# Optimization experiments

Measured on AMD Instinct MI355X. Metric: run time of the kernel, lower is better.

## Reference

```python
import jax, jax.numpy as jnp
import numpy as np

N = 100000   # nodes
E = 1600000  # edges
IN, HID, CLS = 128, 64, 32


def gcn_conv(x, src, dst, W, b, num_nodes):
    """PyG-style GCNConv: out = D^{-1/2} (A+I) D^{-1/2} X W + b."""
    xw = x @ W  # transform first (matches PyG: propagate on transformed feats)
    loop = jnp.arange(num_nodes)
    src_f = jnp.concatenate([src, loop])
    dst_f = jnp.concatenate([dst, loop])
    ones = jnp.ones(src_f.shape[0], dtype=xw.dtype)
    deg = jax.ops.segment_sum(ones, dst_f, num_segments=num_nodes)
    dinv = jnp.where(deg > 0, jax.lax.rsqrt(deg), 0.0)
    norm = dinv[src_f] * dinv[dst_f]            # [E+N]
    msg = xw[src_f] * norm[:, None]             # gather + scale
    out = jax.ops.segment_sum(msg, dst_f, num_segments=num_nodes)
    return out + b


def setup_inputs() -> dict:
    key = jax.random.key(0)
    k = jax.random.split(key, 7)
    x = jax.random.normal(k[0], (N, IN), dtype=jnp.float32)
    edge_index = jax.random.randint(k[1], (2, E), 0, N)
    edge_attr = jax.random.normal(k[2], (E, 1), dtype=jnp.float32)
    W1 = jax.random.normal(k[3], (IN, HID), dtype=jnp.float32) / np.sqrt(IN)
    b1 = jnp.zeros((HID,), dtype=jnp.float32)
    W2 = jax.random.normal(k[4], (HID, CLS), dtype=jnp.float32) / np.sqrt(HID)
    b2 = jnp.zeros((CLS,), dtype=jnp.float32)
    return {"x": x, "edge_index": edge_index, "edge_attr": edge_attr,
            "W1": W1, "b1": b1, "W2": W2, "b2": b2}


def reference(x, edge_index, edge_attr, W1, b1, W2, b2):
    # edge_attr is unpacked by the original forward but unused by GCNConv
    src, dst = edge_index[0], edge_index[1]
    h = jax.nn.relu(gcn_conv(x, src, dst, W1, b1, N))
    return gcn_conv(h, src, dst, W2, b2, N)
```

## Files before the change

### kernel.cpp

```cpp
#include <hip/hip_runtime.h>
#include <hip/hip_fp16.h>

#define N_NODES 100000
#define N_EDGES 1600000
#define IN_F 128
#define HID_F 64
#define CLS_F 32

#define NBKT 512
#define BKT_NODES 196
#define EPB 16384
#define NBLK 98
#define NVAL (NBKT * NBLK)
#define CAPB 5120

typedef short s8v __attribute__((ext_vector_type(8)));
typedef float f4v __attribute__((ext_vector_type(4)));

__device__ __forceinline__ unsigned short f2h(float f) {
    return __half_as_ushort(__float2half_rn(f));
}
__device__ __forceinline__ int packh2(float x, float y) {
    __half2 p = __floats2half2_rn(x, y);
    union { __half2 h; int i; } c; c.h = p; return c.i;
}
__device__ __forceinline__ void acc8(float* a, int4 v) {
    union { int4 i; __half2 h[4]; } c; c.i = v;
#pragma unroll
    for (int j = 0; j < 4; j++) {
        float2 f = __half22float2(c.h[j]);
        a[2 * j] += f.x;
        a[2 * j + 1] += f.y;
    }
}
__device__ __forceinline__ void acc4(float* a, int2 v) {
    union { int2 i; __half2 h[2]; } c; c.i = v;
#pragma unroll
    for (int j = 0; j < 2; j++) {
        float2 f = __half22float2(c.h[j]);
        a[2 * j] += f.x;
        a[2 * j + 1] += f.y;
    }
}


__global__ __launch_bounds__(256) void bucketA_kernel(const int* __restrict__ dst,
                                                      int* __restrict__ bh) {
    __shared__ int h[NBKT];
    for (int i = threadIdx.x; i < NBKT; i += 256) h[i] = 0;
    __syncthreads();
    int e0 = blockIdx.x * EPB;
    int e1 = min(e0 + EPB, N_EDGES);
    for (int e = e0 + threadIdx.x; e < e1; e += 256)
        atomicAdd(&h[dst[e] / BKT_NODES], 1);
    __syncthreads();
    for (int i = threadIdx.x; i < NBKT; i += 256)
        bh[i * NBLK + blockIdx.x] = h[i];
}

__global__ __launch_bounds__(1024) void scan_hist_kernel(int* __restrict__ bh) {
    __shared__ int wsum[16];
    const int CH = (NVAL + 1023) / 1024;
    int t = threadIdx.x;
    int base = t * CH;
    int v[CH];
    int local = 0;
#pragma unroll
    for (int i = 0; i < CH; i++) {
        int idx = base + i;
        int x = (idx < NVAL) ? bh[idx] : 0;
        v[i] = local;
        local += x;
    }
    int lane = t & 63, w = t >> 6;
    int s = local;
#pragma unroll
    for (int d = 1; d < 64; d <<= 1) {
        int u = __shfl_up(s, d);
        if (lane >= d) s += u;
    }
    if (lane == 63) wsum[w] = s;
    __syncthreads();
    int wbase = 0;
    for (int i = 0; i < w; i++) wbase += wsum[i];
    int tbase = wbase + s - local;
#pragma unroll
    for (int i = 0; i < CH; i++) {
        int idx = base + i;
        if (idx < NVAL) bh[idx] = tbase + v[i];
    }
}

__global__ __launch_bounds__(256) void bucketB_kernel(const int* __restrict__ src,
                                                      const int* __restrict__ dst,
                                                      const int* __restrict__ bhScan,
                                                      unsigned* __restrict__ bkt) {
    __shared__ int cur[NBKT];
    for (int i = threadIdx.x; i < NBKT; i += 256)
        cur[i] = bhScan[i * NBLK + blockIdx.x];
    __syncthreads();
    int e0 = blockIdx.x * EPB;
    int e1 = min(e0 + EPB, N_EDGES);
    for (int e = e0 + threadIdx.x; e < e1; e += 256) {
        int d = dst[e];
        int g = d / BKT_NODES;
        unsigned pk = ((unsigned)(d - g * BKT_NODES) << 17) | (unsigned)src[e];
        int pos = atomicAdd(&cur[g], 1);
        bkt[pos] = pk;
    }
}

__global__ __launch_bounds__(256) void sort_bucket_kernel(const int* __restrict__ bhScan,
                                                          const unsigned* __restrict__ bkt,
                                                          int* __restrict__ csr,
                                                          int* __restrict__ off,
                                                          int* __restrict__ endp,
                                                          float* __restrict__ dinv) {
    __shared__ int hist[BKT_NODES];
    __shared__ int loff[BKT_NODES];
    __shared__ int loffB[BKT_NODES];
    __shared__ int wt[4];
    __shared__ int csrS[CAPB];
    int b = blockIdx.x;
    int t = threadIdx.x;
    int s0 = bhScan[b * NBLK];
    int s1 = (b < NBKT - 1) ? bhScan[(b + 1) * NBLK] : N_EDGES;
    int nE = s1 - s0;

    for (int i = t; i < BKT_NODES; i += 256) hist[i] = 0;
    __syncthreads();
    for (int i = t; i < nE; i += 256)
        atomicAdd(&hist[bkt[s0 + i] >> 17], 1);
    __syncthreads();

    int h0 = 0, h1 = 0;
    if (t < 98) { h0 = hist[2 * t]; h1 = hist[2 * t + 1]; }
    int p0 = (h0 + 7) & ~7;
    int p1 = (h1 + 7) & ~7;
    int sum = p0 + p1;
    int lane = t & 63, w = t >> 6;
    int s = sum;
#pragma unroll
    for (int d = 1; d < 64; d <<= 1) {
        int u = __shfl_up(s, d);
        if (lane >= d) s += u;
    }
    if (lane == 63) wt[w] = s;
    __syncthreads();
    int wbase = 0;
    for (int i = 0; i < w; i++) wbase += wt[i];
    int excl = wbase + s - sum;
    if (t < 98) {
        loff[2 * t] = excl;         loffB[2 * t] = excl;
        loff[2 * t + 1] = excl + p0; loffB[2 * t + 1] = excl + p0;
    }
    __syncthreads();

    for (int j = t; j < BKT_NODES; j += 256) {
        int n = b * BKT_NODES + j;
        if (n < N_NODES) {
            int c = hist[j];
            int o = b * CAPB + loff[j];
            off[n] = o;
            endp[n] = o + ((c + 7) & ~7);
            dinv[n] = rsqrtf((float)(c + 1));
        }
    }
    __syncthreads();

    for (int i = t; i < nE; i += 256) {
        unsigned pk = bkt[s0 + i];
        int dl = (int)(pk >> 17);
        int p = atomicAdd(&loff[dl], 1);
        csrS[p] = (int)(pk & 0x1FFFFu);
    }
    __syncthreads();

    for (int j = t; j < BKT_NODES; j += 256) {
        int c = hist[j];
        int bse = loffB[j];
        int pe = bse + ((c + 7) & ~7);
        for (int p = bse + c; p < pe; p++) csrS[p] = N_NODES;
    }
    __syncthreads();

    int padTot = wt[0] + wt[1] + wt[2] + wt[3];
    for (int i = t; i < padTot; i += 256) csr[b * CAPB + i] = csrS[i];
}

#define XBM 64
__global__ __launch_bounds__(256) void xw1_kernel(const float* __restrict__ x,
                                                  const float* __restrict__ W1,
                                                  const float* __restrict__ dinv,
                                                  unsigned short* __restrict__ y1h) {
    __shared__ __align__(16) unsigned short Wb[16 * 64 * 8];
    __shared__ __align__(16) unsigned short xb[XBM][IN_F + 8];

    int tid = threadIdx.x;

    for (int i = tid; i < IN_F * HID_F; i += 256) {
        int k = i >> 6, n = i & 63;
        int kc = k >> 5, kw = k & 31;
        int nt = n >> 4, nl = n & 15;
        int quad = kw >> 3, j = kw & 7;
        Wb[(((kc * 4 + nt) * 64) + quad * 16 + nl) * 8 + j] = f2h(W1[i]);
    }

    int nodeBase = blockIdx.x * XBM;
    {
        int snl = tid >> 2;
        int sk0 = (tid & 3) * 32;
        int n = nodeBase + snl;
#pragma unroll
        for (int kk = 0; kk < 32; kk += 4) {
            float4 v = make_float4(0.f, 0.f, 0.f, 0.f);
            if (n < N_NODES) v = *(const float4*)(x + (size_t)n * IN_F + sk0 + kk);
            ushort4 o;
            o.x = f2h(v.x); o.y = f2h(v.y); o.z = f2h(v.z); o.w = f2h(v.w);
            *(ushort4*)(&xb[snl][sk0 + kk]) = o;
        }
    }
    __syncthreads();

    int wave = tid >> 6, lane = tid & 63;
    int quad = lane >> 4, l15 = lane & 15;
    int rowBase = wave * 16;

    f4v acc[4];
#pragma unroll
    for (int i = 0; i < 4; i++) acc[i] = (f4v){0.f, 0.f, 0.f, 0.f};

#pragma unroll
    for (int kc = 0; kc < 4; kc++) {
        s8v a = *(const s8v*)(&xb[rowBase + l15][kc * 32 + quad * 8]);
#pragma unroll
        for (int nt = 0; nt < 4; nt++) {
            s8v b = *(const s8v*)(&Wb[((kc * 4 + nt) * 64 + lane) * 8]);
            acc[nt] = __builtin_amdgcn_mfma_f32_16x16x32_f16(a, b, acc[nt], 0, 0, 0);
        }
    }

    float dv[4];
    int n0 = nodeBase + rowBase + quad * 4;
#pragma unroll
    for (int r = 0; r < 4; r++)
        dv[r] = (n0 + r < N_NODES) ? dinv[n0 + r] : 0.f;
#pragma unroll
    for (int nt = 0; nt < 4; nt++) {
#pragma unroll
        for (int r = 0; r < 4; r++) {
            int n = n0 + r;
            if (n < N_NODES + 1)
                y1h[(size_t)n * HID_F + nt * 16 + l15] = f2h(acc[nt][r] * dv[r]);
        }
    }
}

__global__ __launch_bounds__(256) void gather1_kernel(
        const int* __restrict__ off, const int* __restrict__ endp,
        const int* __restrict__ csr, const unsigned short* __restrict__ y1h,
        const float* __restrict__ dinv, const float* __restrict__ b1,
        unsigned short* __restrict__ hout) {
    int tid = threadIdx.x;
    int wv = __builtin_amdgcn_readfirstlane(tid >> 6);
    int wave = blockIdx.x * 4 + wv;
    int nA = wave * 2, nB = nA + 1;
    int lane = tid & 63;
    int f = lane & 7;
    int g = lane >> 3;
    int fo = f * 16;

    int offA = off[nA], offB = off[nB];
    int lenA = endp[nA] - offA, lenB = endp[nB] - offB;
    const int* pA = csr + offA + g;
    const int* pB = csr + offB + g;
    const char* yb = (const char*)y1h;

    float aA[8], aB[8];
#pragma unroll
    for (int j = 0; j < 8; j++) { aA[j] = 0.f; aB[j] = 0.f; }

    int lmin = min(lenA, lenB);
    int iA = pA[0], iB = pB[0];
    int t = 0;
    for (; t < lmin; t += 8) {
        int icA = iA, icB = iB;
        iA = pA[t + 8]; iB = pB[t + 8];
        int4 vA = *(const int4*)(yb + (size_t)icA * 128 + fo);
        int4 vB = *(const int4*)(yb + (size_t)icB * 128 + fo);
        acc8(aA, vA); acc8(aB, vB);
    }
    for (; t < lenA; t += 8) {
        int ic = iA; iA = pA[t + 8];
        int4 v = *(const int4*)(yb + (size_t)ic * 128 + fo);
        acc8(aA, v);
    }
    for (int u = lmin; u < lenB; u += 8) {
        int ic = iB; iB = pB[u + 8];
        int4 v = *(const int4*)(yb + (size_t)ic * 128 + fo);
        acc8(aB, v);
    }

#pragma unroll
    for (int m = 8; m <= 32; m <<= 1) {
#pragma unroll
        for (int j = 0; j < 8; j++) {
            aA[j] += __shfl_xor(aA[j], m);
            aB[j] += __shfl_xor(aB[j], m);
        }
    }

    int4 sA = *(const int4*)(yb + (size_t)nA * 128 + fo);
    int4 sB = *(const int4*)(yb + (size_t)nB * 128 + fo);
    acc8(aA, sA); acc8(aB, sB);

    float dvA = dinv[nA], dvB = dinv[nB];
    float4 bl = *(const float4*)(b1 + 8 * f);
    float4 bh4 = *(const float4*)(b1 + 8 * f + 4);
    float bb[8] = {bl.x, bl.y, bl.z, bl.w, bh4.x, bh4.y, bh4.z, bh4.w};
    float hA[8], hB[8];
#pragma unroll
    for (int j = 0; j < 8; j++) {
        hA[j] = fmaxf(aA[j] * dvA + bb[j], 0.f);
        hB[j] = fmaxf(aB[j] * dvB + bb[j], 0.f);
    }
    int4 HA, HB;
    HA.x = packh2(hA[0], hA[1]); HA.y = packh2(hA[2], hA[3]);
    HA.z = packh2(hA[4], hA[5]); HA.w = packh2(hA[6], hA[7]);
    HB.x = packh2(hB[0], hB[1]); HB.y = packh2(hB[2], hB[3]);
    HB.z = packh2(hB[4], hB[5]); HB.w = packh2(hB[6], hB[7]);

    if (lane < 16) {
        int node = (lane < 8) ? nA : nB;
        int4 hv = (lane < 8) ? HA : HB;
        *(int4*)((char*)hout + (size_t)node * 128 + (lane & 7) * 16) = hv;
    }
}

#define YBM 64
__global__ __launch_bounds__(256) void y2_kernel(const unsigned short* __restrict__ h,
                                                 const float* __restrict__ W2,
                                                 const float* __restrict__ dinv,
                                                 unsigned short* __restrict__ y2h) {
    __shared__ __align__(16) unsigned short Wb[2 * 2 * 64 * 8];
    __shared__ __align__(16) unsigned short hb[YBM][HID_F + 8];
    int tid = threadIdx.x;

    for (int i = tid; i < HID_F * CLS_F; i += 256) {
        int k = i >> 5, n = i & 31;
        int kc = k >> 5, kw = k & 31;
        int nt = n >> 4, nl = n & 15;
        int quad = kw >> 3, j = kw & 7;
        Wb[(((kc * 2 + nt) * 64) + quad * 16 + nl) * 8 + j] = f2h(W2[i]);
    }

    int nodeBase = blockIdx.x * YBM;
    {
        int row = tid >> 2, sseg = tid & 3;
        int n = nodeBase + row;
        int4 v0 = {0, 0, 0, 0}, v1 = {0, 0, 0, 0};
        if (n < N_NODES) {
            const char* hp = (const char*)h + (size_t)n * 128 + sseg * 32;
            v0 = *(const int4*)hp;
            v1 = *(const int4*)(hp + 16);
        }
        *(int4*)(&hb[row][sseg * 16]) = v0;
        *(int4*)(&hb[row][sseg * 16 + 8]) = v1;
    }
    __syncthreads();

    int wave = tid >> 6, lane = tid & 63;
    int quad = lane >> 4, l15 = lane & 15;
    int rowBase = wave * 16;

    f4v acc[2];
#pragma unroll
    for (int i = 0; i < 2; i++) acc[i] = (f4v){0.f, 0.f, 0.f, 0.f};

#pragma unroll
    for (int kc = 0; kc < 2; kc++) {
        s8v a = *(const s8v*)(&hb[rowBase + l15][kc * 32 + quad * 8]);
#pragma unroll
        for (int nt = 0; nt < 2; nt++) {
            s8v b = *(const s8v*)(&Wb[((kc * 2 + nt) * 64 + lane) * 8]);
            acc[nt] = __builtin_amdgcn_mfma_f32_16x16x32_f16(a, b, acc[nt], 0, 0, 0);
        }
    }

    float dv[4];
    int n0 = nodeBase + rowBase + quad * 4;
#pragma unroll
    for (int r = 0; r < 4; r++)
        dv[r] = (n0 + r < N_NODES) ? dinv[n0 + r] : 0.f;
#pragma unroll
    for (int nt = 0; nt < 2; nt++) {
#pragma unroll
        for (int r = 0; r < 4; r++) {
            int n = n0 + r;
            if (n < N_NODES + 1)
                y2h[(size_t)n * CLS_F + nt * 16 + l15] = f2h(acc[nt][r] * dv[r]);
        }
    }
}

__global__ __launch_bounds__(256) void gather2_kernel(const int* __restrict__ off,
                                                      const int* __restrict__ endp,
                                                      const int* __restrict__ csr,
                                                      const unsigned short* __restrict__ y2h,
                                                      const float* __restrict__ dinv,
                                                      const float* __restrict__ b2,
                                                      float* __restrict__ out) {
    int tid = threadIdx.x;
    int wv = __builtin_amdgcn_readfirstlane(tid >> 6);
    int wave = blockIdx.x * 4 + wv;
    int nA = wave * 2, nB = nA + 1;
    int lane = tid & 63;
    int f = lane & 7;
    int g = lane >> 3;
    int fo = f * 8;

    int offA = off[nA], offB = off[nB];
    int lenA = endp[nA] - offA, lenB = endp[nB] - offB;
    const int* pA = csr + offA + g;
    const int* pB = csr + offB + g;
    const char* yb = (const char*)y2h;

    float aA[4], aB[4];
#pragma unroll
    for (int j = 0; j < 4; j++) { aA[j] = 0.f; aB[j] = 0.f; }

    int lmin = min(lenA, lenB);
    int iA = pA[0], iB = pB[0];
    int t = 0;
    for (; t < lmin; t += 8) {
        int icA = iA, icB = iB;
        iA = pA[t + 8]; iB = pB[t + 8];
        int2 vA = *(const int2*)(yb + (size_t)icA * 64 + fo);
        int2 vB = *(const int2*)(yb + (size_t)icB * 64 + fo);
        acc4(aA, vA); acc4(aB, vB);
    }
    for (; t < lenA; t += 8) {
        int ic = iA; iA = pA[t + 8];
        int2 v = *(const int2*)(yb + (size_t)ic * 64 + fo);
        acc4(aA, v);
    }
    for (int u = lmin; u < lenB; u += 8) {
        int ic = iB; iB = pB[u + 8];
        int2 v = *(const int2*)(yb + (size_t)ic * 64 + fo);
        acc4(aB, v);
    }

#pragma unroll
    for (int m = 8; m <= 32; m <<= 1) {
#pragma unroll
        for (int j = 0; j < 4; j++) {
            aA[j] += __shfl_xor(aA[j], m);
            aB[j] += __shfl_xor(aB[j], m);
        }
    }

    int2 sA = *(const int2*)(yb + (size_t)nA * 64 + fo);
    int2 sB = *(const int2*)(yb + (size_t)nB * 64 + fo);
    acc4(aA, sA); acc4(aB, sB);

    float dvA = dinv[nA], dvB = dinv[nB];
    float4 b2v = *(const float4*)(b2 + 4 * f);
    float bbv[4] = {b2v.x, b2v.y, b2v.z, b2v.w};
    float4 oA, oB;
    float* oAp = (float*)&oA;
    float* oBp = (float*)&oB;
#pragma unroll
    for (int j = 0; j < 4; j++) {
        oAp[j] = aA[j] * dvA + bbv[j];
        oBp[j] = aB[j] * dvB + bbv[j];
    }
    if (lane < 16) {
        int node = (lane < 8) ? nA : nB;
        float4 ov = (lane < 8) ? oA : oB;
        *(float4*)(out + (size_t)node * CLS_F + (lane & 7) * 4) = ov;
    }
}

extern "C" void kernel_launch(void* const* d_in, const int* in_sizes, int n_in,
                              void* d_out, int out_size, void* d_ws, size_t ws_size,
                              hipStream_t stream) {
    const float* x  = (const float*)d_in[0];
    const int*   ei = (const int*)d_in[1];
    const float* W1 = (const float*)d_in[3];
    const float* b1 = (const float*)d_in[4];
    const float* W2 = (const float*)d_in[5];
    const float* b2 = (const float*)d_in[6];
    float* out = (float*)d_out;

    const int* src = ei;
    const int* dst = ei + N_EDGES;

    char* ws = (char*)d_ws;
    size_t npad = ((size_t)N_NODES * 4 + 255) / 256 * 256;
    float* dinv = (float*)ws;
    int*   off  = (int*)(ws + npad);
    int*   endp = (int*)(ws + 2 * npad);
    int*   bh   = (int*)(ws + 3 * npad);
    int*   csr  = (int*)(ws + 3 * npad + 204800);
    char*  rbase = (char*)csr + (size_t)NBKT * CAPB * 4;
    unsigned* bkt = (unsigned*)rbase;
    unsigned short* y1h = (unsigned short*)rbase;
    unsigned short* y2h = (unsigned short*)(rbase + (size_t)(N_NODES + 1) * HID_F * 2);
    unsigned short* hbuf = (unsigned short*)((char*)y2h + (size_t)(N_NODES + 1) * CLS_F * 2);

    dim3 blk(256);
    bucketA_kernel  <<<dim3(NBLK), blk, 0, stream>>>(dst, bh);
    scan_hist_kernel<<<dim3(1), dim3(1024), 0, stream>>>(bh);
    bucketB_kernel  <<<dim3(NBLK), blk, 0, stream>>>(src, dst, bh, bkt);
    sort_bucket_kernel<<<dim3(NBKT), blk, 0, stream>>>(bh, bkt, csr, off, endp, dinv);
    xw1_kernel      <<<dim3((N_NODES + XBM - 1) / XBM), blk, 0, stream>>>(x, W1, dinv, y1h);
    gather1_kernel  <<<dim3(N_NODES / 8), blk, 0, stream>>>(off, endp, csr, y1h, dinv, b1, hbuf);
    y2_kernel       <<<dim3((N_NODES + YBM) / YBM), blk, 0, stream>>>(hbuf, W2, dinv, y2h);
    gather2_kernel  <<<dim3(N_NODES / 8), blk, 0, stream>>>(off, endp, csr, y2h, dinv, b2, out);
}
```

Measured before the change: 251.0 us.

## Restructure gather loops with prefetch, fdot2 accumulation, merged reductions, vectorized scan

The gather kernels now run a single loop over the longer of the two node neighbour lists. Exhausted lanes read a padding row at index N_NODES, and the next feature row is prefetched one iteration ahead. Half-to-float accumulation uses fdot2 with unit vectors, and the cross-lane reduction packs both nodes into one shuffle stage so half the lanes write. The histogram scan uses int4 loads, and the bucket-pass block count changes from 98 to 64. This relies on the padding row N_NODES being zero in y1h/y2h, and CSR space grows by one bucket to keep reads past the list end in bounds.

After: 271.5 us. 8.2% more time.

```diff
diff --git a/kernel.cpp b/kernel.cpp
--- a/kernel.cpp
+++ b/kernel.cpp
@@ -9,13 +9,14 @@
 
 #define NBKT 512
 #define BKT_NODES 196
-#define EPB 16384
-#define NBLK 98
+#define NBLK 64
+#define EPB 25000
 #define NVAL (NBKT * NBLK)
 #define CAPB 5120
 
 typedef short s8v __attribute__((ext_vector_type(8)));
 typedef float f4v __attribute__((ext_vector_type(4)));
+typedef _Float16 h2v __attribute__((ext_vector_type(2)));
 
 __device__ __forceinline__ unsigned short f2h(float f) {
     return __half_as_ushort(__float2half_rn(f));
@@ -24,23 +25,44 @@
     __half2 p = __floats2half2_rn(x, y);
     union { __half2 h; int i; } c; c.h = p; return c.i;
 }
-__device__ __forceinline__ void acc8(float* a, int4 v) {
+
+__device__ __forceinline__ void dot8(float* a, int4 v) {
+#if __has_builtin(__builtin_amdgcn_fdot2)
+    union { int4 i; h2v h[4]; } c; c.i = v;
+    const h2v E0 = {(_Float16)1.f, (_Float16)0.f};
+    const h2v E1 = {(_Float16)0.f, (_Float16)1.f};
+#pragma unroll
+    for (int j = 0; j < 4; j++) {
+        a[2 * j]     = __builtin_amdgcn_fdot2(c.h[j], E0, a[2 * j], false);
+        a[2 * j + 1] = __builtin_amdgcn_fdot2(c.h[j], E1, a[2 * j + 1], false);
+    }
+#else
     union { int4 i; __half2 h[4]; } c; c.i = v;
 #pragma unroll
     for (int j = 0; j < 4; j++) {
         float2 f = __half22float2(c.h[j]);
-        a[2 * j] += f.x;
-        a[2 * j + 1] += f.y;
-    }
-}
-__device__ __forceinline__ void acc4(float* a, int2 v) {
+        a[2 * j] += f.x; a[2 * j + 1] += f.y;
+    }
+#endif
+}
+__device__ __forceinline__ void dot4(float* a, int2 v) {
+#if __has_builtin(__builtin_amdgcn_fdot2)
+    union { int2 i; h2v h[2]; } c; c.i = v;
+    const h2v E0 = {(_Float16)1.f, (_Float16)0.f};
+    const h2v E1 = {(_Float16)0.f, (_Float16)1.f};
+#pragma unroll
+    for (int j = 0; j < 2; j++) {
+        a[2 * j]     = __builtin_amdgcn_fdot2(c.h[j], E0, a[2 * j], false);
+        a[2 * j + 1] = __builtin_amdgcn_fdot2(c.h[j], E1, a[2 * j + 1], false);
+    }
+#else
     union { int2 i; __half2 h[2]; } c; c.i = v;
 #pragma unroll
     for (int j = 0; j < 2; j++) {
         float2 f = __half22float2(c.h[j]);
-        a[2 * j] += f.x;
-        a[2 * j + 1] += f.y;
-    }
+        a[2 * j] += f.x; a[2 * j + 1] += f.y;
+    }
+#endif
 }
 
 
@@ -60,34 +82,39 @@
 
 __global__ __launch_bounds__(1024) void scan_hist_kernel(int* __restrict__ bh) {
     __shared__ int wsum[16];
-    const int CH = (NVAL + 1023) / 1024;
     int t = threadIdx.x;
-    int base = t * CH;
-    int v[CH];
+    const int4* p = (const int4*)bh + t * 8;
+    int4 w[8];
+#pragma unroll
+    for (int i = 0; i < 8; i++) w[i] = p[i];
     int local = 0;
 #pragma unroll
-    for (int i = 0; i < CH; i++) {
-        int idx = base + i;
-        int x = (idx < NVAL) ? bh[idx] : 0;
-        v[i] = local;
-        local += x;
-    }
-    int lane = t & 63, w = t >> 6;
+    for (int i = 0; i < 8; i++) {
+        int4 v = w[i];
+        int e0 = local;
+        int e1 = e0 + v.x;
+        int e2 = e1 + v.y;
+        int e3 = e2 + v.z;
+        local = e3 + v.w;
+        w[i] = make_int4(e0, e1, e2, e3);
+    }
+    int lane = t & 63, wd = t >> 6;
     int s = local;
 #pragma unroll
     for (int d = 1; d < 64; d <<= 1) {
         int u = __shfl_up(s, d);
         if (lane >= d) s += u;
     }
-    if (lane == 63) wsum[w] = s;
+    if (lane == 63) wsum[wd] = s;
     __syncthreads();
     int wbase = 0;
-    for (int i = 0; i < w; i++) wbase += wsum[i];
+    for (int i = 0; i < wd; i++) wbase += wsum[i];
     int tbase = wbase + s - local;
-#pragma unroll
-    for (int i = 0; i < CH; i++) {
-        int idx = base + i;
-        if (idx < NVAL) bh[idx] = tbase + v[i];
+    int4* q = (int4*)bh + t * 8;
+#pragma unroll
+    for (int i = 0; i < 8; i++) {
+        int4 v = w[i];
+        q[i] = make_int4(v.x + tbase, v.y + tbase, v.z + tbase, v.w + tbase);
     }
 }
 
@@ -272,6 +299,7 @@
 
     int offA = off[nA], offB = off[nB];
     int lenA = endp[nA] - offA, lenB = endp[nB] - offB;
+    int lmax = max(lenA, lenB);
     const int* pA = csr + offA + g;
     const int* pB = csr + offB + g;
     const char* yb = (const char*)y1h;
@@ -280,61 +308,56 @@
 #pragma unroll
     for (int j = 0; j < 8; j++) { aA[j] = 0.f; aB[j] = 0.f; }
 
-    int lmin = min(lenA, lenB);
-    int iA = pA[0], iB = pB[0];
-    int t = 0;
-    for (; t < lmin; t += 8) {
-        int icA = iA, icB = iB;
-        iA = pA[t + 8]; iB = pB[t + 8];
-        int4 vA = *(const int4*)(yb + (size_t)icA * 128 + fo);
-        int4 vB = *(const int4*)(yb + (size_t)icB * 128 + fo);
-        acc8(aA, vA); acc8(aB, vB);
-    }
-    for (; t < lenA; t += 8) {
-        int ic = iA; iA = pA[t + 8];
-        int4 v = *(const int4*)(yb + (size_t)ic * 128 + fo);
-        acc8(aA, v);
-    }
-    for (int u = lmin; u < lenB; u += 8) {
-        int ic = iB; iB = pB[u + 8];
-        int4 v = *(const int4*)(yb + (size_t)ic * 128 + fo);
-        acc8(aB, v);
-    }
-
-#pragma unroll
-    for (int m = 8; m <= 32; m <<= 1) {
-#pragma unroll
-        for (int j = 0; j < 8; j++) {
-            aA[j] += __shfl_xor(aA[j], m);
-            aB[j] += __shfl_xor(aB[j], m);
-        }
-    }
-
-    int4 sA = *(const int4*)(yb + (size_t)nA * 128 + fo);
-    int4 sB = *(const int4*)(yb + (size_t)nB * 128 + fo);
-    acc8(aA, sA); acc8(aB, sB);
+    if (lmax > 0) {
+        int rA = pA[0], rB = pB[0];
+        int iA = (lenA > 0) ? rA : N_NODES;
+        int iB = (lenB > 0) ? rB : N_NODES;
+        int4 vA = *(const int4*)(yb + (size_t)iA * 128 + fo);
+        int4 vB = *(const int4*)(yb + (size_t)iB * 128 + fo);
+        int rA1 = pA[8], rB1 = pB[8];
+        for (int t = 8; t < lmax; t += 8) {
+            int inA = (t < lenA) ? rA1 : N_NODES;
+            int inB = (t < lenB) ? rB1 : N_NODES;
+            int4 nxA = *(const int4*)(yb + (size_t)inA * 128 + fo);
+            int4 nxB = *(const int4*)(yb + (size_t)inB * 128 + fo);
+            rA1 = pA[t + 8]; rB1 = pB[t + 8];
+            dot8(aA, vA); dot8(aB, vB);
+            vA = nxA; vB = nxB;
+        }
+        dot8(aA, vA); dot8(aB, vB);
+    }
+
+    float c8[8];
+#pragma unroll
+    for (int j = 0; j < 8; j++) {
+        float sel = (lane < 32) ? aB[j] : aA[j];
+        float oth = __shfl_xor(sel, 32);
+        c8[j] = ((lane < 32) ? aA[j] : aB[j]) + oth;
+    }
+#pragma unroll
+    for (int m = 8; m <= 16; m <<= 1)
+#pragma unroll
+        for (int j = 0; j < 8; j++) c8[j] += __shfl_xor(c8[j], m);
+
+    int node = (lane < 32) ? nA : nB;
+
+    int4 sv = *(const int4*)(yb + (size_t)node * 128 + fo);
+    dot8(c8, sv);
 
     float dvA = dinv[nA], dvB = dinv[nB];
+    float dvS = (lane < 32) ? dvA : dvB;
     float4 bl = *(const float4*)(b1 + 8 * f);
     float4 bh4 = *(const float4*)(b1 + 8 * f + 4);
     float bb[8] = {bl.x, bl.y, bl.z, bl.w, bh4.x, bh4.y, bh4.z, bh4.w};
-    float hA[8], hB[8];
-#pragma unroll
-    for (int j = 0; j < 8; j++) {
-        hA[j] = fmaxf(aA[j] * dvA + bb[j], 0.f);
-        hB[j] = fmaxf(aB[j] * dvB + bb[j], 0.f);
-    }
-    int4 HA, HB;
-    HA.x = packh2(hA[0], hA[1]); HA.y = packh2(hA[2], hA[3]);
-    HA.z = packh2(hA[4], hA[5]); HA.w = packh2(hA[6], hA[7]);
-    HB.x = packh2(hB[0], hB[1]); HB.y = packh2(hB[2], hB[3]);
-    HB.z = packh2(hB[4], hB[5]); HB.w = packh2(hB[6], hB[7]);
-
-    if (lane < 16) {
-        int node = (lane < 8) ? nA : nB;
-        int4 hv = (lane < 8) ? HA : HB;
-        *(int4*)((char*)hout + (size_t)node * 128 + (lane & 7) * 16) = hv;
-    }
+    float h[8];
+#pragma unroll
+    for (int j = 0; j < 8; j++)
+        h[j] = fmaxf(fmaf(c8[j], dvS, bb[j]), 0.f);
+    int4 H;
+    H.x = packh2(h[0], h[1]); H.y = packh2(h[2], h[3]);
+    H.z = packh2(h[4], h[5]); H.w = packh2(h[6], h[7]);
+    if ((lane & 31) < 8)
+        *(int4*)((char*)hout + (size_t)node * 128 + fo) = H;
 }
 
 #define YBM 64
@@ -421,6 +444,7 @@
 
     int offA = off[nA], offB = off[nB];
     int lenA = endp[nA] - offA, lenB = endp[nB] - offB;
+    int lmax = max(lenA, lenB);
     const int* pA = csr + offA + g;
     const int* pB = csr + offB + g;
     const char* yb = (const char*)y2h;
@@ -429,56 +453,53 @@
 #pragma unroll
     for (int j = 0; j < 4; j++) { aA[j] = 0.f; aB[j] = 0.f; }
 
-    int lmin = min(lenA, lenB);
-    int iA = pA[0], iB = pB[0];
-    int t = 0;
-    for (; t < lmin; t += 8) {
-        int icA = iA, icB = iB;
-        iA = pA[t + 8]; iB = pB[t + 8];
-        int2 vA = *(const int2*)(yb + (size_t)icA * 64 + fo);
-        int2 vB = *(const int2*)(yb + (size_t)icB * 64 + fo);
-        acc4(aA, vA); acc4(aB, vB);
-    }
-    for (; t < lenA; t += 8) {
-        int ic = iA; iA = pA[t + 8];
-        int2 v = *(const int2*)(yb + (size_t)ic * 64 + fo);
-        acc4(aA, v);
-    }
-    for (int u = lmin; u < lenB; u += 8) {
-        int ic = iB; iB = pB[u + 8];
-        int2 v = *(const int2*)(yb + (size_t)ic * 64 + fo);
-        acc4(aB, v);
-    }
-
-#pragma unroll
-    for (int m = 8; m <= 32; m <<= 1) {
-#pragma unroll
-        for (int j = 0; j < 4; j++) {
-            aA[j] += __shfl_xor(aA[j], m);
-            aB[j] += __shfl_xor(aB[j], m);
-        }
-    }
-
-    int2 sA = *(const int2*)(yb + (size_t)nA * 64 + fo);
-    int2 sB = *(const int2*)(yb + (size_t)nB * 64 + fo);
-    acc4(aA, sA); acc4(aB, sB);
+    if (lmax > 0) {
+        int rA = pA[0], rB = pB[0];
+        int iA = (lenA > 0) ? rA : N_NODES;
+        int iB = (lenB > 0) ? rB : N_NODES;
+        int2 vA = *(const int2*)(yb + (size_t)iA * 64 + fo);
+        int2 vB = *(const int2*)(yb + (size_t)iB * 64 + fo);
+        int rA1 = pA[8], rB1 = pB[8];
+        for (int t = 8; t < lmax; t += 8) {
+            int inA = (t < lenA) ? rA1 : N_NODES;
+            int inB = (t < lenB) ? rB1 : N_NODES;
+            int2 nxA = *(const int2*)(yb + (size_t)inA * 64 + fo);
+            int2 nxB = *(const int2*)(yb + (size_t)inB * 64 + fo);
+            rA1 = pA[t + 8]; rB1 = pB[t + 8];
+            dot4(aA, vA); dot4(aB, vB);
+            vA = nxA; vB = nxB;
+        }
+        dot4(aA, vA); dot4(aB, vB);
+    }
+
+    float c4[4];
+#pragma unroll
+    for (int j = 0; j < 4; j++) {
+        float sel = (lane < 32) ? aB[j] : aA[j];
+        float oth = __shfl_xor(sel, 32);
+        c4[j] = ((lane < 32) ? aA[j] : aB[j]) + oth;
+    }
+#pragma unroll
+    for (int m = 8; m <= 16; m <<= 1)
+#pragma unroll
+        for (int j = 0; j < 4; j++) c4[j] += __shfl_xor(c4[j], m);
+
+    int node = (lane < 32) ? nA : nB;
+
+    int2 sv = *(const int2*)(yb + (size_t)node * 64 + fo);
+    dot4(c4, sv);
 
     float dvA = dinv[nA], dvB = dinv[nB];
+    float dvS = (lane < 32) ? dvA : dvB;
     float4 b2v = *(const float4*)(b2 + 4 * f);
     float bbv[4] = {b2v.x, b2v.y, b2v.z, b2v.w};
-    float4 oA, oB;
-    float* oAp = (float*)&oA;
-    float* oBp = (float*)&oB;
-#pragma unroll
-    for (int j = 0; j < 4; j++) {
-        oAp[j] = aA[j] * dvA + bbv[j];
-        oBp[j] = aB[j] * dvB + bbv[j];
-    }
-    if (lane < 16) {
-        int node = (lane < 8) ? nA : nB;
-        float4 ov = (lane < 8) ? oA : oB;
-        *(float4*)(out + (size_t)node * CLS_F + (lane & 7) * 4) = ov;
-    }
+    float4 o4;
+    float* op = (float*)&o4;
+#pragma unroll
+    for (int j = 0; j < 4; j++)
+        op[j] = fmaf(c4[j], dvS, bbv[j]);
+    if ((lane & 31) < 8)
+        *(float4*)(out + (size_t)node * CLS_F + f * 4) = o4;
 }
 
 extern "C" void kernel_launch(void* const* d_in, const int* in_sizes, int n_in,
@@ -502,7 +523,7 @@
     int*   endp = (int*)(ws + 2 * npad);
     int*   bh   = (int*)(ws + 3 * npad);
     int*   csr  = (int*)(ws + 3 * npad + 204800);
-    char*  rbase = (char*)csr + (size_t)NBKT * CAPB * 4;
+    char*  rbase = (char*)csr + (size_t)(NBKT + 1) * CAPB * 4;
     unsigned* bkt = (unsigned*)rbase;
     unsigned short* y1h = (unsigned short*)rbase;
     unsigned short* y2h = (unsigned short*)(rbase + (size_t)(N_NODES + 1) * HID_F * 2);
```
